# Kernel tuning notes

Hardware: AMD Instinct MI355X
Metric: run time of the kernel (lower is better)

Reference implementation:

```python
import jax, jax.numpy as jnp
import numpy as np

B, T, HW, ENC, DEC, ATT, EMB, V = 32, 128, 14, 2048, 512, 512, 512, 10000
P = HW * HW  # num_pixels = 196


def setup_inputs() -> dict:
    key = jax.random.key(0)
    ks = jax.random.split(key, 24)
    s = 0.02
    inp = {
        'bimgs': jax.random.normal(ks[0], (B, HW, HW, ENC), dtype=jnp.float32),
        'bx': jax.random.randint(ks[1], (B, T), 0, V),
        # torch code assumes lengths sorted DESCENDING
        'bxlen': jnp.sort(jax.random.randint(ks[2], (B,), 1, T + 1))[::-1],
        'emb_W': jax.random.normal(ks[3], (V, EMB)) * s,
        'enc_att_W': jax.random.normal(ks[4], (ATT, ENC)) * s,
        'enc_att_b': jnp.zeros((ATT,)),
        'dec_att_W': jax.random.normal(ks[5], (ATT, DEC)) * s,
        'dec_att_b': jnp.zeros((ATT,)),
        'full_att_W': jax.random.normal(ks[6], (1, ATT)) * s,
        'full_att_b': jnp.zeros((1,)),
        'init_h_W': jax.random.normal(ks[7], (DEC, ENC)) * s,
        'init_h_b': jnp.zeros((DEC,)),
        'init_c_W': jax.random.normal(ks[8], (DEC, ENC)) * s,
        'init_c_b': jnp.zeros((DEC,)),
        'f_beta_W': jax.random.normal(ks[9], (ENC, DEC)) * s,
        'f_beta_b': jnp.zeros((ENC,)),
        'W_ih': jax.random.normal(ks[10], (4 * DEC, EMB + ENC)) * s,
        'b_ih': jnp.zeros((4 * DEC,)),
        'W_hh': jax.random.normal(ks[11], (4 * DEC, DEC)) * s,
        'b_hh': jnp.zeros((4 * DEC,)),
        'fc_W': jax.random.normal(ks[12], (V, DEC)) * s,
        'fc_b': jnp.zeros((V,)),
    }
    return inp


def reference(bimgs, bx, bxlen, emb_W, enc_att_W, enc_att_b, dec_att_W, dec_att_b,
              full_att_W, full_att_b, init_h_W, init_h_b, init_c_W, init_c_b,
              f_beta_W, f_beta_b, W_ih, b_ih, W_hh, b_hh, fc_W, fc_b):
    b = bimgs.shape[0]
    imgs = bimgs.reshape(b, -1, bimgs.shape[-1])          # [B,P,enc]
    t_len = bx.shape[-1]
    embeds = emb_W[bx]                                     # [B,T,E]
    mean_img = imgs.mean(axis=1)                           # [B,enc]
    h0 = mean_img @ init_h_W.T + init_h_b                  # [B,dec]
    c0 = mean_img @ init_c_W.T + init_c_b
    # encoder attention projection is time-invariant -> hoist out of the loop
    att1 = imgs @ enc_att_W.T + enc_att_b                  # [B,P,A]
    active_ts = jnp.arange(t_len)[:, None] < bxlen[None, :]  # [T,B]
    emb_ts = embeds.transpose(1, 0, 2)                     # [T,B,E]

    def step(carry, xs):
        h, c = carry
        emb_t, active = xs
        att2 = h @ dec_att_W.T + dec_att_b                 # [B,A]
        e = jax.nn.relu(att1 + att2[:, None, :]) @ full_att_W[0] + full_att_b[0]  # [B,P]
        alpha = jax.nn.softmax(e, axis=1)
        awe = jnp.einsum('bpe,bp->be', imgs, alpha)        # [B,enc]
        gate = jax.nn.sigmoid(h @ f_beta_W.T + f_beta_b)
        x = jnp.concatenate([emb_t, gate * awe], axis=1)   # [B,E+enc]
        # PyTorch LSTMCell: gate order i, f, g, o
        gates = x @ W_ih.T + b_ih + h @ W_hh.T + b_hh
        i_, f_, g_, o_ = jnp.split(gates, 4, axis=1)
        i_ = jax.nn.sigmoid(i_); f_ = jax.nn.sigmoid(f_); o_ = jax.nn.sigmoid(o_)
        g_ = jnp.tanh(g_)
        c_new = f_ * c + i_ * g_
        h_new = o_ * jnp.tanh(c_new)
        preds = h_new @ fc_W.T + fc_b                      # dropout = identity (eval)
        m = active[:, None]
        h2 = jnp.where(m, h_new, h)
        c2 = jnp.where(m, c_new, c)
        return (h2, c2), (jnp.where(m, preds, 0.0), jnp.where(m, alpha, 0.0))

    _, (preds_ts, alphas_ts) = jax.lax.scan(step, (h0, c0), (emb_ts, active_ts))
    predictions = preds_ts.transpose(1, 0, 2)              # [B,T,V]
    alphas = alphas_ts.transpose(1, 0, 2)                  # [B,T,P]
    return predictions, alphas
```

## Files before the change

kernel.cpp:

```cpp
#include <hip/hip_runtime.h>
#include <hip/hip_bf16.h>

#define BB 32
#define TT 128
#define PP 196
#define PPAD 208
#define ENC 2048
#define DEC 512
#define ATT 512
#define EMB 512
#define VV 10000
#define VVP 10240
#define G4 2048
#define KX 2560
#define NWG 256

typedef unsigned short u16;
typedef unsigned int u32;
typedef __attribute__((ext_vector_type(8))) short short8;
typedef __attribute__((ext_vector_type(4))) float f32x4;

__device__ __forceinline__ float bf2f(u16 u) { return __uint_as_float(((u32)u) << 16); }
__device__ __forceinline__ u16 f2bf(float f) {
  u32 x = __float_as_uint(f);
  u32 r = (x + 0x7fffu + ((x >> 16) & 1u)) >> 16;
  return (u16)r;
}
__device__ __forceinline__ void unpack8(uint4 v, float* f) {
  f[0] = __uint_as_float(v.x << 16); f[1] = __uint_as_float(v.x & 0xffff0000u);
  f[2] = __uint_as_float(v.y << 16); f[3] = __uint_as_float(v.y & 0xffff0000u);
  f[4] = __uint_as_float(v.z << 16); f[5] = __uint_as_float(v.z & 0xffff0000u);
  f[6] = __uint_as_float(v.w << 16); f[7] = __uint_as_float(v.w & 0xffff0000u);
}
__device__ __forceinline__ void load8(const float* __restrict__ p, float* f) {
  float4 a = ((const float4*)p)[0];
  float4 b = ((const float4*)p)[1];
  f[0] = a.x; f[1] = a.y; f[2] = a.z; f[3] = a.w;
  f[4] = b.x; f[5] = b.y; f[6] = b.z; f[7] = b.w;
}
__device__ __forceinline__ float sigf(float x) { return 1.0f / (1.0f + __expf(-x)); }
__device__ __forceinline__ short8 ld_frag(const u16* __restrict__ p) {
  union { uint4 u; short8 s; } cv;
  cv.u = *(const uint4*)p;
  return cv.s;
}

__device__ __forceinline__ void ast_f32(float* p, float v) {
  __hip_atomic_store(p, v, __ATOMIC_RELAXED, __HIP_MEMORY_SCOPE_AGENT);
}
__device__ __forceinline__ float ald_f32(const float* p) {
  return __hip_atomic_load((float*)p, __ATOMIC_RELAXED, __HIP_MEMORY_SCOPE_AGENT);
}
__device__ __forceinline__ u32 ald_u32(const u32* p) {
  return __hip_atomic_load((u32*)p, __ATOMIC_RELAXED, __HIP_MEMORY_SCOPE_AGENT);
}
__device__ __forceinline__ void ast_u16(u16* p, u16 v) {
  __hip_atomic_store(p, v, __ATOMIC_RELAXED, __HIP_MEMORY_SCOPE_AGENT);
}

__device__ __forceinline__ int hadr(int b, int d) {
  return ((((b >> 4) << 10) + ((d >> 5) << 6) + (((d >> 3) & 3) << 4) + (b & 15)) << 3) + (d & 7);
}
__device__ __forceinline__ int xadr(int b, int ch) {
  return ((((b >> 4) << 12) + ((ch >> 5) << 6) + (((ch >> 3) & 3) << 4) + (b & 15)) << 3) + (ch & 7);
}

__global__ __launch_bounds__(256) void k_cvt(const float* __restrict__ src, u16* __restrict__ dst, int n) {
  int i0 = (blockIdx.x * 256 + threadIdx.x) * 8;
  if (i0 >= n) return;
  float f[8]; load8(src + i0, f);
  u16 o[8];
#pragma unroll
  for (int u = 0; u < 8; u++) o[u] = f2bf(f[u]);
  *(uint4*)(dst + i0) = *(const uint4*)o;
}

__global__ __launch_bounds__(256) void k_emball(const int* __restrict__ bx,
    const float* __restrict__ embW, u16* __restrict__ xemb) {
  int flat = blockIdx.x * 256 + threadIdx.x;
  int row = flat >> 6;
  int c8 = (flat & 63) * 8;
  int tok = bx[row];
  const float* e = embW + (size_t)tok * EMB + c8;
  float f[8]; load8(e, f);
  u16 o[8];
#pragma unroll
  for (int u = 0; u < 8; u++) o[u] = f2bf(f[u]);
  *(uint4*)(xemb + (size_t)row * EMB + c8) = *(const uint4*)o;
}

__global__ __launch_bounds__(256) void k_timg(const float* __restrict__ imgs, u16* __restrict__ imgsT) {
  int b = blockIdx.x >> 8;
  int sub = blockIdx.x & 255;
  int flat = sub * 256 + threadIdx.x;
  int ch = flat >> 5, pg = flat & 31;
  if (pg >= 26) return;
  u16 o[8];
#pragma unroll
  for (int j = 0; j < 8; j++) {
    int p = pg * 8 + j;
    float v = (p < PP) ? imgs[((size_t)b * PP + p) * ENC + ch] : 0.f;
    o[j] = f2bf(v);
  }
  *(uint4*)(imgsT + ((size_t)b * 2048 + ch) * PPAD + pg * 8) = *(const uint4*)o;
}

__global__ __launch_bounds__(256) void k_mean(const u16* __restrict__ imgs_bf, u16* __restrict__ mean_bf) {
  int b = blockIdx.x >> 2, chunk = blockIdx.x & 3;
  int ch0 = chunk * 512 + threadIdx.x * 2;
  const u32* base = (const u32*)(imgs_bf + (size_t)b * PP * ENC + ch0);
  float a0 = 0.f, a1 = 0.f;
#pragma unroll 4
  for (int p = 0; p < PP; p++) {
    u32 u = base[(size_t)p * (ENC / 2)];
    a0 += __uint_as_float(u << 16);
    a1 += __uint_as_float(u & 0xffff0000u);
  }
  const float inv = 1.0f / PP;
  u16 o[2] = { f2bf(a0 * inv), f2bf(a1 * inv) };
  *(u32*)(mean_bf + b * ENC + ch0) = *(const u32*)o;
}

__global__ __launch_bounds__(64) void k_init2(const u16* __restrict__ W2_bf,
    const float* __restrict__ ihb, const float* __restrict__ icb,
    const u16* __restrict__ mean_bf, u16* __restrict__ h_chunk, float* __restrict__ c) {
  int lane = threadIdx.x;
  int j0 = blockIdx.x * 16;
  int m = lane & 15, quad = lane >> 4;
  const u16* arow = W2_bf + (size_t)(j0 + m) * ENC + quad * 8;
  const u16* xb0 = mean_bf + (size_t)m * ENC + quad * 8;
  const u16* xb1 = mean_bf + (size_t)(16 + m) * ENC + quad * 8;
  f32x4 acc0 = {0.f,0.f,0.f,0.f}, acc1 = {0.f,0.f,0.f,0.f};
  for (int k = 0; k < ENC; k += 32) {
    short8 a = ld_frag(arow + k);
    short8 x0 = ld_frag(xb0 + k);
    short8 x1 = ld_frag(xb1 + k);
    acc0 = __builtin_amdgcn_mfma_f32_16x16x32_bf16(a, x0, acc0, 0, 0, 0);
    acc1 = __builtin_amdgcn_mfma_f32_16x16x32_bf16(a, x1, acc1, 0, 0, 0);
  }
  int jj = j0 + quad * 4;
  int b0 = m, b1 = 16 + m;
#pragma unroll
  for (int r = 0; r < 4; r++) {
    int j = jj + r;
    if (j < 512) {
      float bia = ihb[j];
      h_chunk[hadr(b0, j)] = f2bf(acc0[r] + bia);
      h_chunk[hadr(b1, j)] = f2bf(acc1[r] + bia);
    } else {
      int g = j - 512;
      float bia = icb[g];
      c[b0 * DEC + g] = acc0[r] + bia;
      c[b1 * DEC + g] = acc1[r] + bia;
    }
  }
}

__global__ __launch_bounds__(256) void k_att1(const u16* __restrict__ imgs_bf,
    const u16* __restrict__ encW_bf, const float* __restrict__ encb, u16* __restrict__ att1) {
  int tid = threadIdx.x;
  int wave = tid >> 6, lane = tid & 63;
  int m0 = blockIdx.x * 32;
  int lm = lane & 15, quad = lane >> 4;
  const u16* b0p = imgs_bf + (size_t)(m0 + lm) * ENC + quad * 8;
  const u16* b1p = imgs_bf + (size_t)(m0 + 16 + lm) * ENC + quad * 8;
  const u16* arow = encW_bf + (size_t)(wave * 128 + lm) * ENC + quad * 8;
  f32x4 acc[8][2];
#pragma unroll
  for (int i = 0; i < 8; i++) { acc[i][0] = (f32x4){0.f,0.f,0.f,0.f}; acc[i][1] = (f32x4){0.f,0.f,0.f,0.f}; }
  for (int k = 0; k < ENC; k += 32) {
    short8 B0 = ld_frag(b0p + k);
    short8 B1 = ld_frag(b1p + k);
#pragma unroll
    for (int i = 0; i < 8; i++) {
      short8 A = ld_frag(arow + (size_t)i * 16 * ENC + k);
      acc[i][0] = __builtin_amdgcn_mfma_f32_16x16x32_bf16(A, B0, acc[i][0], 0, 0, 0);
      acc[i][1] = __builtin_amdgcn_mfma_f32_16x16x32_bf16(A, B1, acc[i][1], 0, 0, 0);
    }
  }
#pragma unroll
  for (int i = 0; i < 8; i++) {
    int jb = wave * 128 + i * 16 + quad * 4;
#pragma unroll
    for (int r = 0; r < 4; r++) {
      int j = jb + r;
      float bia = encb[j];
      att1[(size_t)(m0 + lm) * ATT + j]      = f2bf(acc[i][0][r] + bia);
      att1[(size_t)(m0 + 16 + lm) * ATT + j] = f2bf(acc[i][1][r] + bia);
    }
  }
}

__global__ __launch_bounds__(256) void k_zero(unsigned* p, int n) {
  int i = blockIdx.x * 256 + threadIdx.x;
  if (i < n) p[i] = 0u;
}

__device__ __forceinline__ void gbar(u32* arrive, u32* gen, u32 tag, int wg) {
  __syncthreads();
  int tid = threadIdx.x;
  if (wg == 0) {
    if (tid >= 1 && tid < NWG) {
      long sp = 0;
      while (__hip_atomic_load(arrive + tid * 32, __ATOMIC_RELAXED, __HIP_MEMORY_SCOPE_AGENT) < tag) {
        __builtin_amdgcn_s_sleep(1);
        if (++sp > (1L << 24)) break;
      }
    }
    __syncthreads();
    if (tid == 0)
      __hip_atomic_store(gen, tag, __ATOMIC_RELEASE, __HIP_MEMORY_SCOPE_AGENT);
  } else {
    if (tid == 0) {
      __hip_atomic_store(arrive + wg * 32, tag, __ATOMIC_RELEASE, __HIP_MEMORY_SCOPE_AGENT);
      long sp = 0;
      while (__hip_atomic_load(gen, __ATOMIC_RELAXED, __HIP_MEMORY_SCOPE_AGENT) < tag) {
        __builtin_amdgcn_s_sleep(1);
        if (++sp > (1L << 24)) break;
      }
    }
    __syncthreads();
  }
}

__global__ __launch_bounds__(256, 2) void k_mega(
    const int* __restrict__ bxlen,
    const u16* __restrict__ W3,
    const float* __restrict__ decb, const float* __restrict__ fbb,
    const u16* __restrict__ att1, const float* __restrict__ faW, const float* __restrict__ fab,
    const u16* __restrict__ imgsT, const u16* __restrict__ Wih_bf, const u16* __restrict__ xemb,
    const float* __restrict__ bih, const float* __restrict__ bhh,
    u16* __restrict__ h_chunk, float* __restrict__ c_glob, u16* __restrict__ h_hist,
    float* __restrict__ att2, float* __restrict__ gatev, float* __restrict__ hWhh,
    u16* __restrict__ x_aweL, float* __restrict__ e_buf,
    float* __restrict__ out_alphas,
    u32* __restrict__ bar) {
  const int wg = blockIdx.x;
  const int tid = threadIdx.x;
  const int wid = tid >> 6, lane = tid & 63;
  const int m = lane & 15, quad = lane >> 4;
  u32* arrive = bar;
  u32* gen = bar + NWG * 32;

  __shared__ __align__(16) u16 uSX[16384];
  __shared__ float sG[4][16][33];
  __shared__ float sA[512], sW[512];
  __shared__ float sAl[PPAD];
  __shared__ float sR[4], sR2[4];

  const float fab0 = fab[0];
  const int b_p2 = wg >> 3, s_p2 = wg & 7;
  const int len2 = bxlen[b_p2];
  const int b_p3 = b_p2, sub8 = s_p2;
  const int q4 = wg - 224;
  int len4 = 0, b4 = 0, dl4 = 0;
  float c_reg[4] = {0.f, 0.f, 0.f, 0.f};
  if (wg >= 224 && tid < 128) {
    b4 = tid & 31; dl4 = tid >> 5;
    len4 = bxlen[b4];
#pragma unroll
    for (int r = 0; r < 4; r++) c_reg[r] = c_glob[(b4 << 9) + (q4 << 4) + (dl4 << 2) + r];
  }
  for (int i = tid; i < 512; i += 256) sW[i] = faW[i];
  __syncthreads();

  for (int t = 0; t < TT; t++) {
    const u32 base_tag = (u32)t * 4;

    if (wg < 72) {
      {
        const u32* src = (const u32*)h_chunk;
        u32* dstw = (u32*)uSX;
#pragma unroll
        for (int i = 0; i < 8; i++) {
          int cl = (i << 8) + tid;
          int d4i = cl << 2;
          u32 w0 = ald_u32(src + d4i), w1 = ald_u32(src + d4i + 1);
          u32 w2 = ald_u32(src + d4i + 2), w3 = ald_u32(src + d4i + 3);
          uint4 v = {w0, w1, w2, w3};
          *(uint4*)(dstw + d4i) = v;
        }
      }
      __syncthreads();
      int gw = (wg << 2) + wid;
      int j0 = gw << 4;
      const u16* arow = W3 + ((size_t)(j0 + m) << 9) + (quad << 3);
      f32x4 acc0 = {0.f,0.f,0.f,0.f}, acc1 = {0.f,0.f,0.f,0.f};
#pragma unroll 4
      for (int k = 0; k < 16; k++) {
        short8 a = ld_frag(arow + k * 32);
        short8 x0 = ld_frag(uSX + (((k << 6) + lane) << 3));
        short8 x1 = ld_frag(uSX + 8192 + (((k << 6) + lane) << 3));
        acc0 = __builtin_amdgcn_mfma_f32_16x16x32_bf16(a, x0, acc0, 0, 0, 0);
        acc1 = __builtin_amdgcn_mfma_f32_16x16x32_bf16(a, x1, acc1, 0, 0, 0);
      }
      int jj = j0 + (quad << 2);
      int b0 = m, b1 = 16 + m;
      if (j0 < 512) {
#pragma unroll
        for (int r = 0; r < 4; r++) {
          int j = jj + r; float bia = decb[j];
          ast_f32(&att2[(b0 << 9) + j], acc0[r] + bia);
          ast_f32(&att2[(b1 << 9) + j], acc1[r] + bia);
        }
      } else if (j0 < 2560) {
#pragma unroll
        for (int r = 0; r < 4; r++) {
          int g = jj + r - 512; float bia = fbb[g];
          ast_f32(&gatev[(b0 << 11) + g], sigf(acc0[r] + bia));
          ast_f32(&gatev[(b1 << 11) + g], sigf(acc1[r] + bia));
        }
      } else {
#pragma unroll
        for (int r = 0; r < 4; r++) {
          int j = jj + r - 2560;
          ast_f32(&hWhh[(b0 << 11) + j], acc0[r]);
          ast_f32(&hWhh[(b1 << 11) + j], acc1[r]);
        }
      }
    }
    gbar(arrive, gen, base_tag + 1, wg);

    if (t < len2) {
      for (int i = tid; i < 512; i += 256) sA[i] = ald_f32(&att2[(b_p2 << 9) + i]);
      __syncthreads();
      if (tid < 200) {
        int p_loc = tid >> 3, kk = tid & 7;
        int p = s_p2 * 25 + p_loc;
        if (p < PP) {
          const uint4* ar = (const uint4*)(att1 + ((size_t)(b_p2 * PP + p) << 9));
          float acc = 0.f;
          int k0 = kk << 6;
#pragma unroll
          for (int k = k0; k < k0 + 64; k += 8) {
            float af[8]; unpack8(ar[k >> 3], af);
#pragma unroll
            for (int u = 0; u < 8; u++) {
              float v = af[u] + sA[k + u];
              acc += fmaxf(v, 0.f) * sW[k + u];
            }
          }
          acc += __shfl_xor(acc, 1);
          acc += __shfl_xor(acc, 2);
          acc += __shfl_xor(acc, 4);
          if (kk == 0) ast_f32(&e_buf[(b_p2 << 8) + p], acc + fab0);
        }
      }
    }
    gbar(arrive, gen, base_tag + 2, wg);

    {
      if (t < len2) {
        float e_t = (tid < PP) ? ald_f32(&e_buf[(b_p3 << 8) + tid]) : -1e30f;
        float wmax = e_t;
#pragma unroll
        for (int off = 32; off; off >>= 1) wmax = fmaxf(wmax, __shfl_xor(wmax, off));
        if (lane == 0) sR[wid] = wmax;
        __syncthreads();
        float mx = fmaxf(fmaxf(sR[0], sR[1]), fmaxf(sR[2], sR[3]));
        float ex = (tid < PP) ? __expf(e_t - mx) : 0.f;
        float wsum = ex;
#pragma unroll
        for (int off = 32; off; off >>= 1) wsum += __shfl_xor(wsum, off);
        if (lane == 0) sR2[wid] = wsum;
        __syncthreads();
        float inv = 1.0f / (sR2[0] + sR2[1] + sR2[2] + sR2[3]);
        float al = ex * inv;
        if (tid < PP) {
          sAl[tid] = al;
          if (sub8 == 0) out_alphas[((size_t)b_p3 * TT + t) * PP + tid] = al;
        } else if (tid < PPAD) {
          sAl[tid] = 0.f;
        }
        __syncthreads();
        int ch = (sub8 << 8) + tid;
        const uint4* ip = (const uint4*)(imgsT + ((size_t)(b_p3 * 2048 + ch)) * PPAD);
        float acc = 0.f;
#pragma unroll
        for (int pg = 0; pg < 26; pg++) {
          uint4 v = ip[pg];
          float f[8]; unpack8(v, f);
#pragma unroll
          for (int u = 0; u < 8; u++) acc += sAl[pg * 8 + u] * f[u];
        }
        float g = ald_f32(&gatev[(b_p3 << 11) + ch]);
        ast_u16(&x_aweL[xadr(b_p3, ch)], f2bf(g * acc));
      } else {
        if (sub8 == 0 && tid < PP) out_alphas[((size_t)b_p3 * TT + t) * PP + tid] = 0.f;
      }
    }
    gbar(arrive, gen, base_tag + 3, wg);

    if (wg >= 224) {
      f32x4 acc0 = {0.f,0.f,0.f,0.f}, acc1 = {0.f,0.f,0.f,0.f};
      const int row0 = (wid << 9) + (q4 << 4);
      for (int s = 0; s < 5; s++) {
        if (s) __syncthreads();
        if (s == 0) {
#pragma unroll
          for (int i = 0; i < 8; i++) {
            int cl = (i << 8) + tid;
            int plane = cl >> 10, rem = cl & 1023;
            int kk = rem >> 6, l6 = rem & 63;
            int bb = plane * 16 + (l6 & 15);
            int col = (kk << 5) + ((l6 >> 4) << 3);
            uint4 v = *(const uint4*)(xemb + ((size_t)(bb * TT + t) << 9) + col);
            *(uint4*)((u32*)uSX + (cl << 2)) = v;
          }
        } else {
          const u32* src = (const u32*)x_aweL;
#pragma unroll
          for (int i = 0; i < 8; i++) {
            int cl = (i << 8) + tid;
            int plane = cl >> 10, rem = cl & 1023;
            int gi = ((plane << 12) + ((s - 1) << 10) + rem) << 2;
            u32 w0 = ald_u32(src + gi), w1 = ald_u32(src + gi + 1);
            u32 w2 = ald_u32(src + gi + 2), w3 = ald_u32(src + gi + 3);
            uint4 v = {w0, w1, w2, w3};
            *(uint4*)((u32*)uSX + (cl << 2)) = v;
          }
        }
        __syncthreads();
        const u16* arow = Wih_bf + (size_t)(row0 + m) * KX + (s << 9) + (quad << 3);
#pragma unroll 4
        for (int k = 0; k < 16; k++) {
          short8 a = ld_frag(arow + k * 32);
          short8 x0 = ld_frag(uSX + (((k << 6) + lane) << 3));
          short8 x1 = ld_frag(uSX + 8192 + (((k << 6) + lane) << 3));
          acc0 = __builtin_amdgcn_mfma_f32_16x16x32_bf16(a, x0, acc0, 0, 0, 0);
          acc1 = __builtin_amdgcn_mfma_f32_16x16x32_bf16(a, x1, acc1, 0, 0, 0);
        }
      }
#pragma unroll
      for (int r = 0; r < 4; r++) {
        int jl = (quad << 2) + r;
        sG[wid][jl][m] = acc0[r];
        sG[wid][jl][16 + m] = acc1[r];
      }
      __syncthreads();
      if (tid < 128 && t < len4) {
        float pre[4][4];
#pragma unroll
        for (int rr = 0; rr < 4; rr++) {
          int dloc = (dl4 << 2) + rr;
          int d = (q4 << 4) + dloc;
#pragma unroll
          for (int g = 0; g < 4; g++) {
            int j = (g << 9) + d;
            pre[rr][g] = sG[g][dloc][b4] + ald_f32(&hWhh[(b4 << 11) + j]) + bih[j] + bhh[j];
          }
        }
#pragma unroll
        for (int rr = 0; rr < 4; rr++) {
          int d = (q4 << 4) + (dl4 << 2) + rr;
          float i_ = sigf(pre[rr][0]);
          float f_ = sigf(pre[rr][1]);
          float g_ = tanhf(pre[rr][2]);
          float o_ = sigf(pre[rr][3]);
          float cn = f_ * c_reg[rr] + i_ * g_;
          float hn = o_ * tanhf(cn);
          c_reg[rr] = cn;
          u16 hb = f2bf(hn);
          ast_u16(&h_chunk[hadr(b4, d)], hb);
          h_hist[((size_t)b4 * TT + t) * DEC + d] = hb;
        }
      }
    }
    gbar(arrive, gen, base_tag + 4, wg);
  }
}

__global__ __launch_bounds__(256) void k_fcall(const int* __restrict__ bxlen,
    const u16* __restrict__ fcW_bf, const float* __restrict__ fcb,
    const u16* __restrict__ h_hist, float* __restrict__ preds) {
  int tid = threadIdx.x;
  int wave = tid >> 6, lane = tid & 63;
  int m0 = blockIdx.x * 32;
  int jbase = blockIdx.y * 512 + wave * 128;
  int lm = lane & 15, quad = lane >> 4;
  const u16* b0p = h_hist + (size_t)(m0 + lm) * DEC + quad * 8;
  const u16* b1p = h_hist + (size_t)(m0 + 16 + lm) * DEC + quad * 8;
  const u16* arow = fcW_bf + (size_t)(jbase + lm) * DEC + quad * 8;
  f32x4 acc[8][2];
#pragma unroll
  for (int i = 0; i < 8; i++) { acc[i][0] = (f32x4){0.f,0.f,0.f,0.f}; acc[i][1] = (f32x4){0.f,0.f,0.f,0.f}; }
  for (int k = 0; k < DEC; k += 32) {
    short8 B0 = ld_frag(b0p + k);
    short8 B1 = ld_frag(b1p + k);
#pragma unroll
    for (int i = 0; i < 8; i++) {
      short8 A = ld_frag(arow + (size_t)i * 16 * DEC + k);
      acc[i][0] = __builtin_amdgcn_mfma_f32_16x16x32_bf16(A, B0, acc[i][0], 0, 0, 0);
      acc[i][1] = __builtin_amdgcn_mfma_f32_16x16x32_bf16(A, B1, acc[i][1], 0, 0, 0);
    }
  }
  int row0 = m0 + lm, row1 = m0 + 16 + lm;
  bool act0 = ((row0 & 127) < bxlen[row0 >> 7]);
  bool act1 = ((row1 & 127) < bxlen[row1 >> 7]);
#pragma unroll
  for (int i = 0; i < 8; i++) {
    int jb = jbase + i * 16 + quad * 4;
#pragma unroll
    for (int r = 0; r < 4; r++) {
      int j = jb + r;
      if (j < VV) {
        float bia = fcb[j];
        preds[(size_t)row0 * VV + j] = act0 ? (acc[i][0][r] + bia) : 0.f;
        preds[(size_t)row1 * VV + j] = act1 ? (acc[i][1][r] + bia) : 0.f;
      }
    }
  }
}

extern "C" void kernel_launch(void* const* d_in, const int* in_sizes, int n_in,
                              void* d_out, int out_size, void* d_ws, size_t ws_size,
                              hipStream_t stream) {
  const float* imgs = (const float*)d_in[0];
  const int* bx     = (const int*)d_in[1];
  const int* bxlen  = (const int*)d_in[2];
  const float* embW = (const float*)d_in[3];
  const float* encW = (const float*)d_in[4];
  const float* encb = (const float*)d_in[5];
  const float* decW = (const float*)d_in[6];
  const float* decb = (const float*)d_in[7];
  const float* faW  = (const float*)d_in[8];
  const float* fab  = (const float*)d_in[9];
  const float* ihW  = (const float*)d_in[10];
  const float* ihb  = (const float*)d_in[11];
  const float* icW  = (const float*)d_in[12];
  const float* icb  = (const float*)d_in[13];
  const float* fbW  = (const float*)d_in[14];
  const float* fbb  = (const float*)d_in[15];
  const float* Wih  = (const float*)d_in[16];
  const float* bih  = (const float*)d_in[17];
  const float* Whh  = (const float*)d_in[18];
  const float* bhh  = (const float*)d_in[19];
  const float* fcW  = (const float*)d_in[20];
  const float* fcb  = (const float*)d_in[21];

  float* out_preds  = (float*)d_out;
  float* out_alphas = out_preds + (size_t)BB * TT * VV;

  char* wsb = (char*)d_ws;
  size_t off = 0;
  u16* imgs_bf = (u16*)(wsb + off);
  u16* imgsT   = (u16*)(wsb + off);
  off += (size_t)BB * 2048 * PPAD * 2;
  u16* W3_bf   = (u16*)(wsb + off); off += (size_t)4608 * DEC * 2;
  u16* Wih_bf  = (u16*)(wsb + off); off += (size_t)G4 * KX * 2;
  u16* fcW_bf  = (u16*)(wsb + off); off += (size_t)VVP * DEC * 2;
  u16* encW_bf = (u16*)(wsb + off); off += (size_t)ATT * ENC * 2;
  u16* att1    = (u16*)(wsb + off);
  u16* W2_bf   = att1;
  u16* mean_bf = att1 + (size_t)1024 * ENC;
  off += (size_t)BB * PP * ATT * 2;
  u16* xemb    = (u16*)(wsb + off); off += (size_t)BB * TT * EMB * 2;
  u16* h_hist  = (u16*)(wsb + off); off += (size_t)BB * TT * DEC * 2;
  u16* h_chunk = (u16*)(wsb + off); off += (size_t)BB * DEC * 2;
  float* c      = (float*)(wsb + off); off += (size_t)BB * DEC * 4;
  float* att2   = (float*)(wsb + off); off += (size_t)BB * ATT * 4;
  float* gatev  = (float*)(wsb + off); off += (size_t)BB * ENC * 4;
  float* hWhh   = (float*)(wsb + off); off += (size_t)BB * G4 * 4;
  u16* x_aweL   = (u16*)(wsb + off); off += (size_t)BB * ENC * 2;
  float* e_buf  = (float*)(wsb + off); off += (size_t)BB * 256 * 4;
  u32* bar      = (u32*)(wsb + off); off += (size_t)(NWG * 32 + 32) * 4;

  k_cvt<<<(BB * PP * ENC) / 2048, 256, 0, stream>>>(imgs, imgs_bf, BB * PP * ENC);
  k_cvt<<<(DEC * DEC) / 2048, 256, 0, stream>>>(decW, W3_bf, DEC * DEC);
  k_cvt<<<(ENC * DEC) / 2048, 256, 0, stream>>>(fbW, W3_bf + (size_t)DEC * DEC, ENC * DEC);
  k_cvt<<<(G4 * DEC) / 2048, 256, 0, stream>>>(Whh, W3_bf + (size_t)(DEC + ENC) * DEC, G4 * DEC);
  k_cvt<<<(G4 * KX) / 2048, 256, 0, stream>>>(Wih, Wih_bf, G4 * KX);
  k_cvt<<<(VV * DEC) / 2048, 256, 0, stream>>>(fcW, fcW_bf, VV * DEC);
  k_cvt<<<(ATT * ENC) / 2048, 256, 0, stream>>>(encW, encW_bf, ATT * ENC);
  k_cvt<<<(DEC * ENC) / 2048, 256, 0, stream>>>(ihW, W2_bf, DEC * ENC);
  k_cvt<<<(DEC * ENC) / 2048, 256, 0, stream>>>(icW, W2_bf + (size_t)DEC * ENC, DEC * ENC);
  k_emball<<<(BB * TT * EMB / 8) / 256, 256, 0, stream>>>(bx, embW, xemb);

  k_mean<<<BB * 4, 256, 0, stream>>>(imgs_bf, mean_bf);
  k_init2<<<64, 64, 0, stream>>>(W2_bf, ihb, icb, mean_bf, h_chunk, c);
  k_att1<<<(BB * PP) / 32, 256, 0, stream>>>(imgs_bf, encW_bf, encb, att1);
  k_timg<<<32 * 256, 256, 0, stream>>>(imgs, imgsT);
  k_zero<<<(NWG * 32 + 32 + 255) / 256, 256, 0, stream>>>(bar, NWG * 32 + 32);

  k_mega<<<NWG, 256, 0, stream>>>(bxlen, W3_bf, decb, fbb, att1, faW, fab,
                                  imgsT, Wih_bf, xemb, bih, bhh,
                                  h_chunk, c, h_hist, att2, gatev, hWhh,
                                  x_aweL, e_buf, out_alphas, bar);

  k_fcall<<<dim3((BB * TT) / 32, 20), 256, 0, stream>>>(bxlen, fcW_bf, fcb, h_hist, out_preds);
}
```

Measured before the change: 7.576 ms.

## Merge attention score and softmax phases, precompute embedding gate GEMM, decentralize barrier

Each workgroup now computes the full 196 attention scores for its batch row locally, so the separate score phase, the e_buf buffer and one grid barrier per timestep go away (three barriers instead of four). The embedding part of the LSTM input projection is precomputed for all timesteps by a new MFMA GEMM kernel before the recurrent loop, which removes one K-slice from the per-step gate GEMM. The barrier is replaced with a flat all-to-all arrival array polled by one wave, dropping the master workgroup round-trip. In exchange, the score work is duplicated 8x per batch row, there is an extra bf16 gate buffer in memory, and every workgroup now polls all arrivals.

```diff
diff --git a/kernel.cpp b/kernel.cpp
--- a/kernel.cpp
+++ b/kernel.cpp
@@ -191,36 +191,68 @@
   }
 }
 
+__global__ __launch_bounds__(256) void k_gemb(const u16* __restrict__ Wih_bf,
+    const u16* __restrict__ xemb, u16* __restrict__ ge) {
+  int tid = threadIdx.x;
+  int wave = tid >> 6, lane = tid & 63;
+  int m0 = blockIdx.x * 32;
+  int jbase = blockIdx.y * 512 + wave * 128;
+  int lm = lane & 15, quad = lane >> 4;
+  const u16* b0p = xemb + ((size_t)(m0 + lm) << 9) + (quad << 3);
+  const u16* b1p = xemb + ((size_t)(m0 + 16 + lm) << 9) + (quad << 3);
+  const u16* arow = Wih_bf + (size_t)(jbase + lm) * KX + (quad << 3);
+  f32x4 acc[8][2];
+#pragma unroll
+  for (int i = 0; i < 8; i++) { acc[i][0] = (f32x4){0.f,0.f,0.f,0.f}; acc[i][1] = (f32x4){0.f,0.f,0.f,0.f}; }
+  for (int k = 0; k < 512; k += 32) {
+    short8 B0 = ld_frag(b0p + k);
+    short8 B1 = ld_frag(b1p + k);
+#pragma unroll
+    for (int i = 0; i < 8; i++) {
+      short8 A = ld_frag(arow + (size_t)i * 16 * KX + k);
+      acc[i][0] = __builtin_amdgcn_mfma_f32_16x16x32_bf16(A, B0, acc[i][0], 0, 0, 0);
+      acc[i][1] = __builtin_amdgcn_mfma_f32_16x16x32_bf16(A, B1, acc[i][1], 0, 0, 0);
+    }
+  }
+#pragma unroll
+  for (int i = 0; i < 8; i++) {
+#pragma unroll
+    for (int r = 0; r < 4; r++) {
+      int j = jbase + i * 16 + quad * 4 + r;
+      int d = j & 511, g9 = j >> 9;
+      int jq = ((d >> 2) << 4) + (g9 << 2) + (d & 3);
+      ge[((size_t)(m0 + lm)) * G4 + jq]      = f2bf(acc[i][0][r]);
+      ge[((size_t)(m0 + 16 + lm)) * G4 + jq] = f2bf(acc[i][1][r]);
+    }
+  }
+}
+
 __global__ __launch_bounds__(256) void k_zero(unsigned* p, int n) {
   int i = blockIdx.x * 256 + threadIdx.x;
   if (i < n) p[i] = 0u;
 }
 
-__device__ __forceinline__ void gbar(u32* arrive, u32* gen, u32 tag, int wg) {
+__device__ __forceinline__ void dbar(u32* arr, u32 tag) {
   __syncthreads();
   int tid = threadIdx.x;
-  if (wg == 0) {
-    if (tid >= 1 && tid < NWG) {
-      long sp = 0;
-      while (__hip_atomic_load(arrive + tid * 32, __ATOMIC_RELAXED, __HIP_MEMORY_SCOPE_AGENT) < tag) {
-        __builtin_amdgcn_s_sleep(1);
-        if (++sp > (1L << 24)) break;
-      }
-    }
-    __syncthreads();
-    if (tid == 0)
-      __hip_atomic_store(gen, tag, __ATOMIC_RELEASE, __HIP_MEMORY_SCOPE_AGENT);
-  } else {
-    if (tid == 0) {
-      __hip_atomic_store(arrive + wg * 32, tag, __ATOMIC_RELEASE, __HIP_MEMORY_SCOPE_AGENT);
-      long sp = 0;
-      while (__hip_atomic_load(gen, __ATOMIC_RELAXED, __HIP_MEMORY_SCOPE_AGENT) < tag) {
-        __builtin_amdgcn_s_sleep(1);
-        if (++sp > (1L << 24)) break;
-      }
-    }
-    __syncthreads();
-  }
+  if (tid == 0) {
+    __hip_atomic_store(arr + blockIdx.x, tag, __ATOMIC_RELAXED, __HIP_MEMORY_SCOPE_AGENT);
+  }
+  if (tid < 64) {
+    int i0 = tid << 2;
+    long sp = 0;
+    while (true) {
+      u32 a0 = ald_u32(arr + i0);
+      u32 a1 = ald_u32(arr + i0 + 1);
+      u32 a2 = ald_u32(arr + i0 + 2);
+      u32 a3 = ald_u32(arr + i0 + 3);
+      bool ok = (a0 >= tag) && (a1 >= tag) && (a2 >= tag) && (a3 >= tag);
+      if (__ballot(ok) == ~0ULL) break;
+      __builtin_amdgcn_s_sleep(2);
+      if (++sp > (1L << 21)) break;
+    }
+  }
+  __syncthreads();
 }
 
 __global__ __launch_bounds__(256, 2) void k_mega(
@@ -228,19 +260,17 @@
     const u16* __restrict__ W3,
     const float* __restrict__ decb, const float* __restrict__ fbb,
     const u16* __restrict__ att1, const float* __restrict__ faW, const float* __restrict__ fab,
-    const u16* __restrict__ imgsT, const u16* __restrict__ Wih_bf, const u16* __restrict__ xemb,
+    const u16* __restrict__ imgsT, const u16* __restrict__ Wih_bf, const u16* __restrict__ ge,
     const float* __restrict__ bih, const float* __restrict__ bhh,
     u16* __restrict__ h_chunk, float* __restrict__ c_glob, u16* __restrict__ h_hist,
     float* __restrict__ att2, float* __restrict__ gatev, float* __restrict__ hWhh,
-    u16* __restrict__ x_aweL, float* __restrict__ e_buf,
+    u16* __restrict__ x_aweL,
     float* __restrict__ out_alphas,
     u32* __restrict__ bar) {
   const int wg = blockIdx.x;
   const int tid = threadIdx.x;
   const int wid = tid >> 6, lane = tid & 63;
   const int m = lane & 15, quad = lane >> 4;
-  u32* arrive = bar;
-  u32* gen = bar + NWG * 32;
 
   __shared__ __align__(16) u16 uSX[16384];
   __shared__ float sG[4][16][33];
@@ -249,9 +279,8 @@
   __shared__ float sR[4], sR2[4];
 
   const float fab0 = fab[0];
-  const int b_p2 = wg >> 3, s_p2 = wg & 7;
-  const int len2 = bxlen[b_p2];
-  const int b_p3 = b_p2, sub8 = s_p2;
+  const int b_g = wg >> 3, s_g = wg & 7;
+  const int len_g = bxlen[b_g];
   const int q4 = wg - 224;
   int len4 = 0, b4 = 0, dl4 = 0;
   float c_reg[4] = {0.f, 0.f, 0.f, 0.f};
@@ -265,7 +294,7 @@
   __syncthreads();
 
   for (int t = 0; t < TT; t++) {
-    const u32 base_tag = (u32)t * 4;
+    const u32 base_tag = (u32)t * 3;
 
     if (wg < 72) {
       {
@@ -319,101 +348,76 @@
         }
       }
     }
-    gbar(arrive, gen, base_tag + 1, wg);
-
-    if (t < len2) {
-      for (int i = tid; i < 512; i += 256) sA[i] = ald_f32(&att2[(b_p2 << 9) + i]);
+    dbar(bar, base_tag + 1);
+
+    if (t < len_g) {
+      for (int i = tid; i < 512; i += 256) sA[i] = ald_f32(&att2[(b_g << 9) + i]);
+      float gch = ald_f32(&gatev[(b_g << 11) + (s_g << 8) + tid]);
       __syncthreads();
-      if (tid < 200) {
-        int p_loc = tid >> 3, kk = tid & 7;
-        int p = s_p2 * 25 + p_loc;
-        if (p < PP) {
-          const uint4* ar = (const uint4*)(att1 + ((size_t)(b_p2 * PP + p) << 9));
-          float acc = 0.f;
-          int k0 = kk << 6;
-#pragma unroll
-          for (int k = k0; k < k0 + 64; k += 8) {
-            float af[8]; unpack8(ar[k >> 3], af);
-#pragma unroll
-            for (int u = 0; u < 8; u++) {
-              float v = af[u] + sA[k + u];
-              acc += fmaxf(v, 0.f) * sW[k + u];
-            }
+      float e_t = -1e30f;
+      if (tid < PP) {
+        const uint4* ar = (const uint4*)(att1 + ((size_t)(b_g * PP + tid) << 9));
+        float acc = 0.f;
+#pragma unroll 8
+        for (int k = 0; k < 512; k += 8) {
+          float af[8]; unpack8(ar[k >> 3], af);
+#pragma unroll
+          for (int u = 0; u < 8; u++) {
+            float v = af[u] + sA[k + u];
+            acc += fmaxf(v, 0.f) * sW[k + u];
           }
-          acc += __shfl_xor(acc, 1);
-          acc += __shfl_xor(acc, 2);
-          acc += __shfl_xor(acc, 4);
-          if (kk == 0) ast_f32(&e_buf[(b_p2 << 8) + p], acc + fab0);
-        }
-      }
-    }
-    gbar(arrive, gen, base_tag + 2, wg);
-
-    {
-      if (t < len2) {
-        float e_t = (tid < PP) ? ald_f32(&e_buf[(b_p3 << 8) + tid]) : -1e30f;
-        float wmax = e_t;
-#pragma unroll
-        for (int off = 32; off; off >>= 1) wmax = fmaxf(wmax, __shfl_xor(wmax, off));
-        if (lane == 0) sR[wid] = wmax;
-        __syncthreads();
-        float mx = fmaxf(fmaxf(sR[0], sR[1]), fmaxf(sR[2], sR[3]));
-        float ex = (tid < PP) ? __expf(e_t - mx) : 0.f;
-        float wsum = ex;
-#pragma unroll
-        for (int off = 32; off; off >>= 1) wsum += __shfl_xor(wsum, off);
-        if (lane == 0) sR2[wid] = wsum;
-        __syncthreads();
-        float inv = 1.0f / (sR2[0] + sR2[1] + sR2[2] + sR2[3]);
-        float al = ex * inv;
-        if (tid < PP) {
-          sAl[tid] = al;
-          if (sub8 == 0) out_alphas[((size_t)b_p3 * TT + t) * PP + tid] = al;
-        } else if (tid < PPAD) {
-          sAl[tid] = 0.f;
-        }
-        __syncthreads();
-        int ch = (sub8 << 8) + tid;
-        const uint4* ip = (const uint4*)(imgsT + ((size_t)(b_p3 * 2048 + ch)) * PPAD);
-        float acc = 0.f;
-#pragma unroll
-        for (int pg = 0; pg < 26; pg++) {
-          uint4 v = ip[pg];
-          float f[8]; unpack8(v, f);
-#pragma unroll
-          for (int u = 0; u < 8; u++) acc += sAl[pg * 8 + u] * f[u];
-        }
-        float g = ald_f32(&gatev[(b_p3 << 11) + ch]);
-        ast_u16(&x_aweL[xadr(b_p3, ch)], f2bf(g * acc));
-      } else {
-        if (sub8 == 0 && tid < PP) out_alphas[((size_t)b_p3 * TT + t) * PP + tid] = 0.f;
-      }
-    }
-    gbar(arrive, gen, base_tag + 3, wg);
+        }
+        e_t = acc + fab0;
+      }
+      float wmax = e_t;
+#pragma unroll
+      for (int off = 32; off; off >>= 1) wmax = fmaxf(wmax, __shfl_xor(wmax, off));
+      if (lane == 0) sR[wid] = wmax;
+      __syncthreads();
+      float mx = fmaxf(fmaxf(sR[0], sR[1]), fmaxf(sR[2], sR[3]));
+      float ex = (tid < PP) ? __expf(e_t - mx) : 0.f;
+      float wsum = ex;
+#pragma unroll
+      for (int off = 32; off; off >>= 1) wsum += __shfl_xor(wsum, off);
+      if (lane == 0) sR2[wid] = wsum;
+      __syncthreads();
+      float inv = 1.0f / (sR2[0] + sR2[1] + sR2[2] + sR2[3]);
+      float al = ex * inv;
+      if (tid < PP) {
+        sAl[tid] = al;
+        if (s_g == 0) out_alphas[((size_t)b_g * TT + t) * PP + tid] = al;
+      } else if (tid < PPAD) {
+        sAl[tid] = 0.f;
+      }
+      __syncthreads();
+      int ch = (s_g << 8) + tid;
+      const uint4* ip = (const uint4*)(imgsT + ((size_t)(b_g * 2048 + ch)) * PPAD);
+      float acc = 0.f;
+#pragma unroll
+      for (int pg = 0; pg < 26; pg++) {
+        uint4 v = ip[pg];
+        float f[8]; unpack8(v, f);
+#pragma unroll
+        for (int u = 0; u < 8; u++) acc += sAl[pg * 8 + u] * f[u];
+      }
+      ast_u16(&x_aweL[xadr(b_g, ch)], f2bf(gch * acc));
+    } else {
+      if (s_g == 0 && tid < PP) out_alphas[((size_t)b_g * TT + t) * PP + tid] = 0.f;
+    }
+    dbar(bar, base_tag + 2);
 
     if (wg >= 224) {
       f32x4 acc0 = {0.f,0.f,0.f,0.f}, acc1 = {0.f,0.f,0.f,0.f};
       const int row0 = (wid << 9) + (q4 << 4);
-      for (int s = 0; s < 5; s++) {
+      for (int s = 0; s < 4; s++) {
         if (s) __syncthreads();
-        if (s == 0) {
+        {
+          const u32* src = (const u32*)x_aweL;
 #pragma unroll
           for (int i = 0; i < 8; i++) {
             int cl = (i << 8) + tid;
             int plane = cl >> 10, rem = cl & 1023;
-            int kk = rem >> 6, l6 = rem & 63;
-            int bb = plane * 16 + (l6 & 15);
-            int col = (kk << 5) + ((l6 >> 4) << 3);
-            uint4 v = *(const uint4*)(xemb + ((size_t)(bb * TT + t) << 9) + col);
-            *(uint4*)((u32*)uSX + (cl << 2)) = v;
-          }
-        } else {
-          const u32* src = (const u32*)x_aweL;
-#pragma unroll
-          for (int i = 0; i < 8; i++) {
-            int cl = (i << 8) + tid;
-            int plane = cl >> 10, rem = cl & 1023;
-            int gi = ((plane << 12) + ((s - 1) << 10) + rem) << 2;
+            int gi = ((plane << 12) + (s << 10) + rem) << 2;
             u32 w0 = ald_u32(src + gi), w1 = ald_u32(src + gi + 1);
             u32 w2 = ald_u32(src + gi + 2), w3 = ald_u32(src + gi + 3);
             uint4 v = {w0, w1, w2, w3};
@@ -421,7 +425,7 @@
           }
         }
         __syncthreads();
-        const u16* arow = Wih_bf + (size_t)(row0 + m) * KX + (s << 9) + (quad << 3);
+        const u16* arow = Wih_bf + (size_t)(row0 + m) * KX + 512 + (s << 9) + (quad << 3);
 #pragma unroll 4
         for (int k = 0; k < 16; k++) {
           short8 a = ld_frag(arow + k * 32);
@@ -439,6 +443,12 @@
       }
       __syncthreads();
       if (tid < 128 && t < len4) {
+        const u16* gep = ge + ((size_t)b4 * TT + t) * G4 + ((((q4 << 2) + dl4)) << 4);
+        uint4 gv0 = *(const uint4*)gep;
+        uint4 gv1 = *(const uint4*)(gep + 8);
+        float gef[16];
+        unpack8(gv0, gef);
+        unpack8(gv1, gef + 8);
         float pre[4][4];
 #pragma unroll
         for (int rr = 0; rr < 4; rr++) {
@@ -447,7 +457,8 @@
 #pragma unroll
           for (int g = 0; g < 4; g++) {
             int j = (g << 9) + d;
-            pre[rr][g] = sG[g][dloc][b4] + ald_f32(&hWhh[(b4 << 11) + j]) + bih[j] + bhh[j];
+            pre[rr][g] = sG[g][dloc][b4] + gef[(g << 2) + rr]
+                       + ald_f32(&hWhh[(b4 << 11) + j]) + bih[j] + bhh[j];
           }
         }
 #pragma unroll
@@ -466,7 +477,7 @@
         }
       }
     }
-    gbar(arrive, gen, base_tag + 4, wg);
+    dbar(bar, base_tag + 3);
   }
 }
 
@@ -556,14 +567,14 @@
   off += (size_t)BB * PP * ATT * 2;
   u16* xemb    = (u16*)(wsb + off); off += (size_t)BB * TT * EMB * 2;
   u16* h_hist  = (u16*)(wsb + off); off += (size_t)BB * TT * DEC * 2;
+  u16* ge      = (u16*)(wsb + off); off += (size_t)BB * TT * G4 * 2;
   u16* h_chunk = (u16*)(wsb + off); off += (size_t)BB * DEC * 2;
   float* c      = (float*)(wsb + off); off += (size_t)BB * DEC * 4;
   float* att2   = (float*)(wsb + off); off += (size_t)BB * ATT * 4;
   float* gatev  = (float*)(wsb + off); off += (size_t)BB * ENC * 4;
   float* hWhh   = (float*)(wsb + off); off += (size_t)BB * G4 * 4;
   u16* x_aweL   = (u16*)(wsb + off); off += (size_t)BB * ENC * 2;
-  float* e_buf  = (float*)(wsb + off); off += (size_t)BB * 256 * 4;
-  u32* bar      = (u32*)(wsb + off); off += (size_t)(NWG * 32 + 32) * 4;
+  u32* bar      = (u32*)(wsb + off); off += (size_t)512 * 4;
 
   k_cvt<<<(BB * PP * ENC) / 2048, 256, 0, stream>>>(imgs, imgs_bf, BB * PP * ENC);
   k_cvt<<<(DEC * DEC) / 2048, 256, 0, stream>>>(decW, W3_bf, DEC * DEC);
@@ -575,17 +586,18 @@
   k_cvt<<<(DEC * ENC) / 2048, 256, 0, stream>>>(ihW, W2_bf, DEC * ENC);
   k_cvt<<<(DEC * ENC) / 2048, 256, 0, stream>>>(icW, W2_bf + (size_t)DEC * ENC, DEC * ENC);
   k_emball<<<(BB * TT * EMB / 8) / 256, 256, 0, stream>>>(bx, embW, xemb);
+  k_gemb<<<dim3((BB * TT) / 32, 4), 256, 0, stream>>>(Wih_bf, xemb, ge);
 
   k_mean<<<BB * 4, 256, 0, stream>>>(imgs_bf, mean_bf);
   k_init2<<<64, 64, 0, stream>>>(W2_bf, ihb, icb, mean_bf, h_chunk, c);
   k_att1<<<(BB * PP) / 32, 256, 0, stream>>>(imgs_bf, encW_bf, encb, att1);
   k_timg<<<32 * 256, 256, 0, stream>>>(imgs, imgsT);
-  k_zero<<<(NWG * 32 + 32 + 255) / 256, 256, 0, stream>>>(bar, NWG * 32 + 32);
+  k_zero<<<2, 256, 0, stream>>>(bar, 512);
 
   k_mega<<<NWG, 256, 0, stream>>>(bxlen, W3_bf, decb, fbb, att1, faW, fab,
-                                  imgsT, Wih_bf, xemb, bih, bhh,
+                                  imgsT, Wih_bf, ge, bih, bhh,
                                   h_chunk, c, h_hist, att2, gatev, hWhh,
-                                  x_aweL, e_buf, out_alphas, bar);
+                                  x_aweL, out_alphas, bar);
 
   k_fcall<<<dim3((BB * TT) / 32, 20), 256, 0, stream>>>(bxlen, fcW_bf, fcb, h_hist, out_preds);
 }
```

Measured after the change: 11.35 ms. 1.5x slower.
